# Performance work log

Measured on AMD Instinct MI355X. Metric: run time of the kernel, lower is better.

The kernel has to match this reference:

```python
import jax, jax.numpy as jnp
import numpy as np

FM = 64            # feature_maps
PASS_STEPS = 3
OUT_BITS = 16


def _linear(x, w, b):
    return x @ w + b


def _mlp(x, w1, b1, w2, b2):
    return _linear(jax.nn.relu(_linear(x, w1, b1)), w2, b2)


def setup_inputs() -> dict:
    key = jax.random.key(0)
    ks = jax.random.split(key, 20)
    VAR, CON, NNZ = 100000, 50000, 2000000

    def w(k, i, o):
        return jax.random.normal(k, (i, o), dtype=jnp.float32) * 0.05

    inp = {
        "row_idx": jax.random.randint(ks[0], (NNZ,), 0, VAR),
        "col_idx": jax.random.randint(ks[1], (NNZ,), 0, CON),
        "adj_vals": jax.random.normal(ks[2], (NNZ,), dtype=jnp.float32),
        "conditions_values": jax.random.normal(ks[3], (CON,), dtype=jnp.float32),
        "var_count": VAR,
        "const_count": CON,
        # prepare_cond: 1 -> 2*FM -> FM
        "pc_w1": w(ks[4], 1, 2 * FM), "pc_b1": jnp.zeros((2 * FM,), jnp.float32),
        "pc_w2": w(ks[5], 2 * FM, FM), "pc_b2": jnp.zeros((FM,), jnp.float32),
        # constraint_update: 2*FM -> 2*FM -> FM
        "cu_w1": w(ks[6], 2 * FM, 2 * FM), "cu_b1": jnp.zeros((2 * FM,), jnp.float32),
        "cu_w2": w(ks[7], 2 * FM, FM), "cu_b2": jnp.zeros((FM,), jnp.float32),
        # variable_update: 2*FM -> 2*FM -> FM
        "vu_w1": w(ks[8], 2 * FM, 2 * FM), "vu_b1": jnp.zeros((2 * FM,), jnp.float32),
        "vu_w2": w(ks[9], 2 * FM, FM), "vu_b2": jnp.zeros((FM,), jnp.float32),
        # output: FM -> 2*FM -> OUT_BITS
        "out_w1": w(ks[10], FM, 2 * FM), "out_b1": jnp.zeros((2 * FM,), jnp.float32),
        "out_w2": w(ks[11], 2 * FM, OUT_BITS), "out_b2": jnp.zeros((OUT_BITS,), jnp.float32),
    }
    return inp


def reference(row_idx, col_idx, adj_vals, conditions_values, var_count, const_count,
              pc_w1, pc_b1, pc_w2, pc_b2,
              cu_w1, cu_b1, cu_w2, cu_b2,
              vu_w1, vu_b1, vu_w2, vu_b2,
              out_w1, out_b1, out_w2, out_b2):
    vals = jnp.abs(adj_vals)                                   # [nnz]
    variables = jnp.ones((var_count, FM), dtype=jnp.float32)   # [V, FM]
    constraints = _mlp(conditions_values[:, None], pc_w1, pc_b1, pc_w2, pc_b2)  # [C, FM]

    for _ in range(PASS_STEPS):
        # var -> const: A^T @ variables  (gather rows, scatter-add to cols)
        v2c = jax.ops.segment_sum(vals[:, None] * variables[row_idx],
                                  col_idx, num_segments=const_count)   # [C, FM]
        constraints = _mlp(jnp.concatenate([constraints, v2c], axis=-1),
                           cu_w1, cu_b1, cu_w2, cu_b2)
        # const -> var: A @ constraints
        c2v = jax.ops.segment_sum(vals[:, None] * constraints[col_idx],
                                  row_idx, num_segments=var_count)     # [V, FM]
        variables = _mlp(jnp.concatenate([variables, c2v], axis=-1),
                         vu_w1, vu_b1, vu_w2, vu_b2)

    return jax.nn.sigmoid(_mlp(variables, out_w1, out_b1, out_w2, out_b2))  # [V, OUT_BITS]
```

## Files before the change

### kernel.cpp

```cpp
#include <hip/hip_runtime.h>
#include <hip/hip_fp16.h>

typedef unsigned int uint;

#define GB_D 64
#define MS_CH 8192
#define BS_CAP 6912

using h8  = __attribute__((ext_vector_type(8))) _Float16;
using h4  = __attribute__((ext_vector_type(4))) _Float16;
using f4v = __attribute__((ext_vector_type(4))) float;

__device__ __forceinline__ float4 ld4(const float* p) { return *reinterpret_cast<const float4*>(p); }
__device__ __forceinline__ void st4(float* p, float4 v) { *reinterpret_cast<float4*>(p) = v; }
__device__ __forceinline__ void fma4(float4& a, float s, const float4 w) {
    a.x = fmaf(s, w.x, a.x); a.y = fmaf(s, w.y, a.y);
    a.z = fmaf(s, w.z, a.z); a.w = fmaf(s, w.w, a.w);
}
__device__ __forceinline__ uint pk2(float a, float b) {
    __half2 h = __floats2half2_rn(a, b);
    return *reinterpret_cast<uint*>(&h);
}

__global__ __launch_bounds__(256) void k_bhist(const int* __restrict__ row, const int* __restrict__ col,
                                               int nnz, int* __restrict__ bcnt, int nbc, int nbt) {
    extern __shared__ int ls[];
    for (int b = threadIdx.x; b < nbt; b += blockDim.x) ls[b] = 0;
    __syncthreads();
    int i0 = blockIdx.x * blockDim.x + threadIdx.x;
    int stride = gridDim.x * blockDim.x;
    for (int i = i0; i < nnz; i += stride) {
        atomicAdd(&ls[col[i] >> 6], 1);
        atomicAdd(&ls[nbc + (row[i] >> 6)], 1);
    }
    __syncthreads();
    for (int b = threadIdx.x; b < nbt; b += blockDim.x) {
        int c = ls[b];
        if (c) atomicAdd(&bcnt[b], c);
    }
}

__global__ __launch_bounds__(1024) void k_bscan(const int* __restrict__ cnt, int n,
                                                int* __restrict__ ptr, int* __restrict__ nxt) {
    __shared__ int wsum[17];
    __shared__ int carry, tot;
    if (threadIdx.x == 0) carry = 0;
    __syncthreads();
    int lane = threadIdx.x & 63;
    int wid  = threadIdx.x >> 6;
    for (int base = 0; base < n; base += 1024) {
        int idx = base + (int)threadIdx.x;
        int v = (idx < n) ? cnt[idx] : 0;
        int inc = v;
        #pragma unroll
        for (int off = 1; off < 64; off <<= 1) {
            int t = __shfl_up(inc, (unsigned)off, 64);
            if (lane >= off) inc += t;
        }
        if (lane == 63) wsum[wid] = inc;
        __syncthreads();
        if (threadIdx.x == 0) {
            int s = 0;
            for (int w = 0; w < 16; w++) { int t = wsum[w]; wsum[w] = s; s += t; }
            tot = s;
        }
        __syncthreads();
        int excl = carry + wsum[wid] + (inc - v);
        if (idx < n) { ptr[idx] = excl; nxt[idx] = excl; }
        __syncthreads();
        if (threadIdx.x == 0) carry += tot;
        __syncthreads();
    }
    if (threadIdx.x == 0) ptr[n] = carry;
}

__global__ __launch_bounds__(256) void k_mpsplit(const int* __restrict__ row, const int* __restrict__ col,
                                                 const float* __restrict__ adj, int nnz,
                                                 int* __restrict__ bnxt, int2* __restrict__ pack,
                                                 int nbc, int nbt) {
    extern __shared__ int ls[];
    const int t = threadIdx.x;
    for (int b = t; b < nbt; b += 256) ls[b] = 0;
    __syncthreads();
    const int start = blockIdx.x * MS_CH;
    const int end = min(start + MS_CH, nnz);
    for (int i = start + t; i < end; i += 256) {
        atomicAdd(&ls[col[i] >> 6], 1);
        atomicAdd(&ls[nbc + (row[i] >> 6)], 1);
    }
    __syncthreads();
    for (int b = t; b < nbt; b += 256) {
        int c = ls[b];
        ls[b] = c ? atomicAdd(&bnxt[b], c) : 0;
    }
    __syncthreads();
    for (int i = start + t; i < end; i += 256) {
        int r = row[i], c = col[i];
        int vb = __float_as_int(fabsf(adj[i]));
        int p1 = atomicAdd(&ls[c >> 6], 1);
        pack[p1] = make_int2(((c & 63) << 20) | r, vb);
        int p2 = atomicAdd(&ls[nbc + (r >> 6)], 1);
        pack[p2] = make_int2(((r & 63) << 20) | c, vb);
    }
}

__global__ __launch_bounds__(256) void k_bsort(const int* __restrict__ bptr, int2* __restrict__ pack,
                                               int* __restrict__ dptr_c, int C,
                                               int* __restrict__ dptr_v, int V, int nbc) {
    __shared__ int2 ebuf[BS_CAP];
    __shared__ int h[GB_D];
    __shared__ int cur[GB_D];
    const int b = blockIdx.x, t = threadIdx.x;
    const int s = bptr[b], e = bptr[b + 1];
    const int n = min(e - s, BS_CAP);
    if (t < GB_D) h[t] = 0;
    __syncthreads();
    for (int i = t; i < n; i += 256) {
        int2 ed = pack[s + i];
        ebuf[i] = ed;
        atomicAdd(&h[((uint)ed.x) >> 20], 1);
    }
    __syncthreads();
    if (t < GB_D) {
        int v = h[t];
        int inc = v;
        #pragma unroll
        for (int off = 1; off < 64; off <<= 1) {
            int u = __shfl_up(inc, (unsigned)off, 64);
            if (t >= off) inc += u;
        }
        int excl = inc - v;
        cur[t] = excl;
        const bool isC = (b < nbc);
        const int base = (isC ? b : b - nbc) << 6;
        const int nd   = isC ? C : V;
        int* dp        = isC ? dptr_c : dptr_v;
        const int d = base + t;
        if (d < nd) dp[d] = s + excl;
        if (d == nd - 1) dp[nd] = s + n;
    }
    __syncthreads();
    for (int i = t; i < n; i += 256) {
        int2 ed = ebuf[i];
        int p = atomicAdd(&cur[((uint)ed.x) >> 20], 1);
        pack[s + p] = make_int2(ed.x & 0xFFFFF, ed.y);
    }
}

__global__ __launch_bounds__(256) void k_gather(const int* __restrict__ dptr,
                                                const int2* __restrict__ es,
                                                const __half* __restrict__ sfeat,
                                                float* __restrict__ dmsg, int n) {
    int wid = (int)((blockIdx.x * blockDim.x + threadIdx.x) >> 6);
    int lane = threadIdx.x & 63;
    int nw = (int)((gridDim.x * blockDim.x) >> 6);
    for (int d = wid; d < n; d += nw) {
        int s = dptr[d], e = dptr[d + 1];
        float a0 = 0.f, a1 = 0.f, a2 = 0.f, a3 = 0.f;
        float a4 = 0.f, a5 = 0.f, a6 = 0.f, a7 = 0.f;
        int i = s;
        for (; i + 7 < e; i += 8) {
            int2 e0 = es[i],     e1 = es[i + 1], e2 = es[i + 2], e3 = es[i + 3];
            int2 e4 = es[i + 4], e5 = es[i + 5], e6 = es[i + 6], e7 = es[i + 7];
            a0 = fmaf(__int_as_float(e0.y), __half2float(sfeat[(size_t)e0.x * 64 + lane]), a0);
            a1 = fmaf(__int_as_float(e1.y), __half2float(sfeat[(size_t)e1.x * 64 + lane]), a1);
            a2 = fmaf(__int_as_float(e2.y), __half2float(sfeat[(size_t)e2.x * 64 + lane]), a2);
            a3 = fmaf(__int_as_float(e3.y), __half2float(sfeat[(size_t)e3.x * 64 + lane]), a3);
            a4 = fmaf(__int_as_float(e4.y), __half2float(sfeat[(size_t)e4.x * 64 + lane]), a4);
            a5 = fmaf(__int_as_float(e5.y), __half2float(sfeat[(size_t)e5.x * 64 + lane]), a5);
            a6 = fmaf(__int_as_float(e6.y), __half2float(sfeat[(size_t)e6.x * 64 + lane]), a6);
            a7 = fmaf(__int_as_float(e7.y), __half2float(sfeat[(size_t)e7.x * 64 + lane]), a7);
        }
        for (; i + 1 < e; i += 2) {
            int2 e0 = es[i], e1 = es[i + 1];
            a0 = fmaf(__int_as_float(e0.y), __half2float(sfeat[(size_t)e0.x * 64 + lane]), a0);
            a1 = fmaf(__int_as_float(e1.y), __half2float(sfeat[(size_t)e1.x * 64 + lane]), a1);
        }
        if (i < e) {
            int2 e0 = es[i];
            a0 = fmaf(__int_as_float(e0.y), __half2float(sfeat[(size_t)e0.x * 64 + lane]), a0);
        }
        dmsg[(size_t)d * 64 + lane] = ((a0 + a1) + (a2 + a3)) + ((a4 + a5) + (a6 + a7));
    }
}

__global__ __launch_bounds__(256) void k_ones2(float4* p, int n4, uint4* ph, int n4h) {
    int i0 = blockIdx.x * blockDim.x + threadIdx.x;
    int stride = gridDim.x * blockDim.x;
    float4 one = make_float4(1.f, 1.f, 1.f, 1.f);
    uint4 oneh = make_uint4(0x3C003C00u, 0x3C003C00u, 0x3C003C00u, 0x3C003C00u);
    for (int i = i0; i < n4; i += stride) p[i] = one;
    for (int i = i0; i < n4h; i += stride) ph[i] = oneh;
}

__global__ __launch_bounds__(256) void k_pc2(const float* __restrict__ cond, float* __restrict__ constraints,
                                             __half* __restrict__ conh, int C,
                                             const float* __restrict__ w1, const float* __restrict__ b1,
                                             const float* __restrict__ w2, const float* __restrict__ b2) {
    __shared__ float hs[64][132];
    __shared__ float cs[64];
    const int t = threadIdx.x;
    const int base = blockIdx.x * 64;
    const int rem = C - base;

    if (t < 64) cs[t] = (t < rem) ? cond[base + t] : 0.f;
    __syncthreads();

    #pragma unroll
    for (int j = 0; j < 32; j++) {
        int idx = j * 256 + t;
        int k = idx & 127, row = idx >> 7;
        hs[row][k] = fmaxf(fmaf(cs[row], w1[k], b1[k]), 0.f);
    }
    __syncthreads();

    const int tx2 = t & 15, ty2 = t >> 4;
    float4 bb = ld4(b2 + tx2 * 4);
    float4 acc[4] = { bb, bb, bb, bb };
    const float* w2p = w2 + tx2 * 4;
    #pragma unroll 4
    for (int k = 0; k < 128; k++) {
        float4 w = ld4(w2p + k * 64);
        fma4(acc[0], hs[ty2 * 4 + 0][k], w);
        fma4(acc[1], hs[ty2 * 4 + 1][k], w);
        fma4(acc[2], hs[ty2 * 4 + 2][k], w);
        fma4(acc[3], hs[ty2 * 4 + 3][k], w);
    }
    #pragma unroll
    for (int r = 0; r < 4; r++) {
        int row = ty2 * 4 + r;
        if (row < rem) {
            st4(&constraints[(size_t)(base + row) * 64 + tx2 * 4], acc[r]);
            uint2 o;
            o.x = pk2(acc[r].x, acc[r].y);
            o.y = pk2(acc[r].z, acc[r].w);
            *(uint2*)(conh + (size_t)(base + row) * 64 + tx2 * 4) = o;
        }
    }
}

__global__ __launch_bounds__(256) void k_mlp3(float* __restrict__ feat, const float* __restrict__ msg,
                                              __half* __restrict__ mirror, int n,
                                              const float* __restrict__ w1, const float* __restrict__ b1,
                                              const float* __restrict__ w2, const float* __restrict__ b2) {
    __shared__ _Float16 xh[64][136];
    __shared__ _Float16 xl[64][136];
    const int t = threadIdx.x;
    const int base = blockIdx.x * 64;
    const int rem = n - base;
    const int wv = t >> 6;
    const int la = t & 15;
    const int lb = (t & 63) >> 4;

    {
        const float4* f4p = (const float4*)(feat + (size_t)base * 64);
        const float4* m4p = (const float4*)(msg + (size_t)base * 64);
        #pragma unroll
        for (int j = 0; j < 8; j++) {
            int idx = j * 256 + t;
            int row = idx >> 5;
            int q   = idx & 31;
            float4 v = make_float4(0.f, 0.f, 0.f, 0.f);
            if (row < rem) v = (q < 16) ? f4p[row * 16 + q] : m4p[row * 16 + (q - 16)];
            int k = (q < 16) ? q * 4 : 64 + (q - 16) * 4;
            h4 hi, lo;
            hi[0] = (_Float16)v.x; lo[0] = (_Float16)(v.x - (float)hi[0]);
            hi[1] = (_Float16)v.y; lo[1] = (_Float16)(v.y - (float)hi[1]);
            hi[2] = (_Float16)v.z; lo[2] = (_Float16)(v.z - (float)hi[2]);
            hi[3] = (_Float16)v.w; lo[3] = (_Float16)(v.w - (float)hi[3]);
            *(h4*)&xh[row][k] = hi;
            *(h4*)&xl[row][k] = lo;
        }
    }

    h8 B1[2][4];
    h8 B2[4];
    #pragma unroll
    for (int nn = 0; nn < 2; nn++) {
        int col = wv * 32 + nn * 16 + la;
        #pragma unroll
        for (int kc = 0; kc < 4; kc++) {
            int kb = kc * 32 + lb * 8;
            h8 bb;
            #pragma unroll
            for (int j = 0; j < 8; j++) bb[j] = (_Float16)w1[(kb + j) * 128 + col];
            B1[nn][kc] = bb;
        }
    }
    {
        int col = wv * 16 + la;
        #pragma unroll
        for (int kc = 0; kc < 4; kc++) {
            int kb = kc * 32 + lb * 8;
            h8 bb;
            #pragma unroll
            for (int j = 0; j < 8; j++) bb[j] = (_Float16)w2[(kb + j) * 64 + col];
            B2[kc] = bb;
        }
    }
    const float b1v0 = b1[wv * 32 + la];
    const float b1v1 = b1[wv * 32 + 16 + la];
    const float b2v  = b2[wv * 16 + la];

    __syncthreads();

    f4v acc[4][2];
    #pragma unroll
    for (int r = 0; r < 4; r++) {
        f4v z = {0.f, 0.f, 0.f, 0.f};
        acc[r][0] = z; acc[r][1] = z;
    }
    #pragma unroll
    for (int r = 0; r < 4; r++) {
        h8 Ah[4], Al[4];
        #pragma unroll
        for (int kc = 0; kc < 4; kc++) {
            Ah[kc] = *(const h8*)&xh[r * 16 + la][kc * 32 + lb * 8];
            Al[kc] = *(const h8*)&xl[r * 16 + la][kc * 32 + lb * 8];
        }
        #pragma unroll
        for (int nn = 0; nn < 2; nn++) {
            #pragma unroll
            for (int kc = 0; kc < 4; kc++) {
                acc[r][nn] = __builtin_amdgcn_mfma_f32_16x16x32_f16(Ah[kc], B1[nn][kc], acc[r][nn], 0, 0, 0);
                acc[r][nn] = __builtin_amdgcn_mfma_f32_16x16x32_f16(Al[kc], B1[nn][kc], acc[r][nn], 0, 0, 0);
            }
        }
    }
    __syncthreads();

    #pragma unroll
    for (int r = 0; r < 4; r++) {
        #pragma unroll
        for (int nn = 0; nn < 2; nn++) {
            const float bv = nn ? b1v1 : b1v0;
            const int col = wv * 32 + nn * 16 + la;
            #pragma unroll
            for (int i = 0; i < 4; i++) {
                float h = fmaxf(acc[r][nn][i] + bv, 0.f);
                int row = r * 16 + lb * 4 + i;
                _Float16 hh = (_Float16)h;
                xh[row][col] = hh;
                xl[row][col] = (_Float16)(h - (float)hh);
            }
        }
    }
    __syncthreads();

    f4v acc2[4];
    #pragma unroll
    for (int r = 0; r < 4; r++) { f4v z = {0.f, 0.f, 0.f, 0.f}; acc2[r] = z; }
    #pragma unroll
    for (int r = 0; r < 4; r++) {
        h8 Ah[4], Al[4];
        #pragma unroll
        for (int kc = 0; kc < 4; kc++) {
            Ah[kc] = *(const h8*)&xh[r * 16 + la][kc * 32 + lb * 8];
            Al[kc] = *(const h8*)&xl[r * 16 + la][kc * 32 + lb * 8];
        }
        #pragma unroll
        for (int kc = 0; kc < 4; kc++) {
            acc2[r] = __builtin_amdgcn_mfma_f32_16x16x32_f16(Ah[kc], B2[kc], acc2[r], 0, 0, 0);
            acc2[r] = __builtin_amdgcn_mfma_f32_16x16x32_f16(Al[kc], B2[kc], acc2[r], 0, 0, 0);
        }
    }

    {
        const int col = wv * 16 + la;
        #pragma unroll
        for (int r = 0; r < 4; r++) {
            #pragma unroll
            for (int i = 0; i < 4; i++) {
                int row = r * 16 + lb * 4 + i;
                if (row < rem) {
                    float y = acc2[r][i] + b2v;
                    size_t idx = (size_t)(base + row) * 64 + col;
                    feat[idx] = y;
                    mirror[idx] = __float2half_rn(y);
                }
            }
        }
    }
}

__global__ __launch_bounds__(256) void k_out3(const float* __restrict__ vars, float* __restrict__ out, int V,
                                              const float* __restrict__ w1, const float* __restrict__ b1,
                                              const float* __restrict__ w2, const float* __restrict__ b2) {
    __shared__ _Float16 xh[64][136];
    __shared__ _Float16 xl[64][136];
    const int t = threadIdx.x;
    const int base = blockIdx.x * 64;
    const int rem = V - base;
    const int wv = t >> 6;
    const int la = t & 15;
    const int lb = (t & 63) >> 4;

    {
        const float4* v4p = (const float4*)(vars + (size_t)base * 64);
        #pragma unroll
        for (int j = 0; j < 4; j++) {
            int idx = j * 256 + t;
            int row = idx >> 4;
            int q   = idx & 15;
            float4 v = make_float4(0.f, 0.f, 0.f, 0.f);
            if (row < rem) v = v4p[row * 16 + q];
            int k = q * 4;
            h4 hi, lo;
            hi[0] = (_Float16)v.x; lo[0] = (_Float16)(v.x - (float)hi[0]);
            hi[1] = (_Float16)v.y; lo[1] = (_Float16)(v.y - (float)hi[1]);
            hi[2] = (_Float16)v.z; lo[2] = (_Float16)(v.z - (float)hi[2]);
            hi[3] = (_Float16)v.w; lo[3] = (_Float16)(v.w - (float)hi[3]);
            *(h4*)&xh[row][k] = hi;
            *(h4*)&xl[row][k] = lo;
        }
    }

    h8 B1[2][2];
    h8 B2[4];
    #pragma unroll
    for (int nn = 0; nn < 2; nn++) {
        int col = wv * 32 + nn * 16 + la;
        #pragma unroll
        for (int kc = 0; kc < 2; kc++) {
            int kb = kc * 32 + lb * 8;
            h8 bb;
            #pragma unroll
            for (int j = 0; j < 8; j++) bb[j] = (_Float16)w1[(kb + j) * 128 + col];
            B1[nn][kc] = bb;
        }
    }
    {
        int col = la;
        #pragma unroll
        for (int kc = 0; kc < 4; kc++) {
            int kb = kc * 32 + lb * 8;
            h8 bb;
            #pragma unroll
            for (int j = 0; j < 8; j++) bb[j] = (_Float16)w2[(kb + j) * 16 + col];
            B2[kc] = bb;
        }
    }
    const float b1v0 = b1[wv * 32 + la];
    const float b1v1 = b1[wv * 32 + 16 + la];
    const float b2v  = b2[la];

    __syncthreads();

    f4v acc[4][2];
    #pragma unroll
    for (int r = 0; r < 4; r++) {
        f4v z = {0.f, 0.f, 0.f, 0.f};
        acc[r][0] = z; acc[r][1] = z;
    }
    #pragma unroll
    for (int r = 0; r < 4; r++) {
        h8 Ah[2], Al[2];
        #pragma unroll
        for (int kc = 0; kc < 2; kc++) {
            Ah[kc] = *(const h8*)&xh[r * 16 + la][kc * 32 + lb * 8];
            Al[kc] = *(const h8*)&xl[r * 16 + la][kc * 32 + lb * 8];
        }
        #pragma unroll
        for (int nn = 0; nn < 2; nn++) {
            #pragma unroll
            for (int kc = 0; kc < 2; kc++) {
                acc[r][nn] = __builtin_amdgcn_mfma_f32_16x16x32_f16(Ah[kc], B1[nn][kc], acc[r][nn], 0, 0, 0);
                acc[r][nn] = __builtin_amdgcn_mfma_f32_16x16x32_f16(Al[kc], B1[nn][kc], acc[r][nn], 0, 0, 0);
            }
        }
    }
    __syncthreads();

    #pragma unroll
    for (int r = 0; r < 4; r++) {
        #pragma unroll
        for (int nn = 0; nn < 2; nn++) {
            const float bv = nn ? b1v1 : b1v0;
            const int col = wv * 32 + nn * 16 + la;
            #pragma unroll
            for (int i = 0; i < 4; i++) {
                float h = fmaxf(acc[r][nn][i] + bv, 0.f);
                int row = r * 16 + lb * 4 + i;
                _Float16 hh = (_Float16)h;
                xh[row][col] = hh;
                xl[row][col] = (_Float16)(h - (float)hh);
            }
        }
    }
    __syncthreads();

    f4v acc2 = {0.f, 0.f, 0.f, 0.f};
    {
        h8 Ah[4], Al[4];
        #pragma unroll
        for (int kc = 0; kc < 4; kc++) {
            Ah[kc] = *(const h8*)&xh[wv * 16 + la][kc * 32 + lb * 8];
            Al[kc] = *(const h8*)&xl[wv * 16 + la][kc * 32 + lb * 8];
        }
        #pragma unroll
        for (int kc = 0; kc < 4; kc++) {
            acc2 = __builtin_amdgcn_mfma_f32_16x16x32_f16(Ah[kc], B2[kc], acc2, 0, 0, 0);
            acc2 = __builtin_amdgcn_mfma_f32_16x16x32_f16(Al[kc], B2[kc], acc2, 0, 0, 0);
        }
    }

    #pragma unroll
    for (int i = 0; i < 4; i++) {
        int row = wv * 16 + lb * 4 + i;
        if (row < rem) {
            float y = acc2[i] + b2v;
            out[(size_t)(base + row) * 16 + la] = 1.f / (1.f + __expf(-y));
        }
    }
}


extern "C" void kernel_launch(void* const* d_in, const int* in_sizes, int n_in,
                              void* d_out, int out_size, void* d_ws, size_t ws_size,
                              hipStream_t stream) {
    const int*   row_idx = (const int*)d_in[0];
    const int*   col_idx = (const int*)d_in[1];
    const float* adj     = (const float*)d_in[2];
    const float* cond    = (const float*)d_in[3];
    const float* pc_w1  = (const float*)d_in[6];
    const float* pc_b1  = (const float*)d_in[7];
    const float* pc_w2  = (const float*)d_in[8];
    const float* pc_b2  = (const float*)d_in[9];
    const float* cu_w1  = (const float*)d_in[10];
    const float* cu_b1  = (const float*)d_in[11];
    const float* cu_w2  = (const float*)d_in[12];
    const float* cu_b2  = (const float*)d_in[13];
    const float* vu_w1  = (const float*)d_in[14];
    const float* vu_b1  = (const float*)d_in[15];
    const float* vu_w2  = (const float*)d_in[16];
    const float* vu_b2  = (const float*)d_in[17];
    const float* out_w1 = (const float*)d_in[18];
    const float* out_b1 = (const float*)d_in[19];
    const float* out_w2 = (const float*)d_in[20];
    const float* out_b2 = (const float*)d_in[21];

    const int NNZ = in_sizes[0];
    const int C   = in_sizes[3];
    const int V   = out_size / 16;

    const int NBc = (C + GB_D - 1) / GB_D;
    const int NBv = (V + GB_D - 1) / GB_D;
    const int NBT = NBc + NBv;

    float* out = (float*)d_out;

    char* wsb = (char*)d_ws;
    size_t off = 0;
    auto carve = [&](size_t bytes) -> void* {
        void* p = wsb + off;
        off = (off + bytes + 255) & ~(size_t)255;
        return p;
    };
    float*  variables   = (float*)carve((size_t)V * 64 * 4);
    float*  constraints = (float*)carve((size_t)C * 64 * 4);
    float*  v2c         = (float*)carve((size_t)C * 64 * 4);
    float*  c2v         = (float*)carve((size_t)V * 64 * 4);
    __half* var_h       = (__half*)carve((size_t)V * 64 * 2);
    __half* con_h       = (__half*)carve((size_t)C * 64 * 2);
    int2*   pack        = (int2*)carve((size_t)2 * NNZ * 8);
    int*    bcnt        = (int*)carve((size_t)NBT * 4);
    int*    bptr        = (int*)carve((size_t)(NBT + 1) * 4);
    int*    bnxt        = (int*)carve((size_t)NBT * 4);
    int*    dptr_c      = (int*)carve((size_t)(C + 1) * 4);
    int*    dptr_v      = (int*)carve((size_t)(V + 1) * 4);
    (void)ws_size; (void)n_in;

    const size_t shmem = (size_t)NBT * 4;

    hipMemsetAsync(bcnt, 0, (size_t)NBT * 4, stream);
    k_bhist<<<256, 256, shmem, stream>>>(row_idx, col_idx, NNZ, bcnt, NBc, NBT);
    k_bscan<<<1, 1024, 0, stream>>>(bcnt, NBT, bptr, bnxt);
    k_mpsplit<<<(NNZ + MS_CH - 1) / MS_CH, 256, shmem, stream>>>(row_idx, col_idx, adj, NNZ,
                                                                 bnxt, pack, NBc, NBT);
    k_bsort<<<NBT, 256, 0, stream>>>(bptr, pack, dptr_c, C, dptr_v, V, NBc);

    k_ones2<<<2048, 256, 0, stream>>>((float4*)variables, V * 16, (uint4*)var_h, V * 8);
    k_pc2<<<(C + 63) / 64, 256, 0, stream>>>(cond, constraints, con_h, C, pc_w1, pc_b1, pc_w2, pc_b2);

    for (int p = 0; p < 3; p++) {
        k_gather<<<2048, 256, 0, stream>>>(dptr_c, pack, var_h, v2c, C);
        k_mlp3<<<(C + 63) / 64, 256, 0, stream>>>(constraints, v2c, con_h, C, cu_w1, cu_b1, cu_w2, cu_b2);
        k_gather<<<2048, 256, 0, stream>>>(dptr_v, pack, con_h, c2v, V);
        k_mlp3<<<(V + 63) / 64, 256, 0, stream>>>(variables, c2v, var_h, V, vu_w1, vu_b1, vu_w2, vu_b2);
    }

    k_out3<<<(V + 63) / 64, 256, 0, stream>>>(variables, out, V, out_w1, out_b1, out_w2, out_b2);
}
```

Measured before the change: 823.2 us.

## Skip first-pass v2c gather via row-sum of weights and drop ones init

Because the variables start as all ones, the first var-to-constraint message equals the per-constraint sum of |adj| weights. That sum is now computed inside the bucket-sort kernel and written straight into v2c, so the first gather and the ones-fill kernel are no longer needed. The variable-update MLP gets a flag that substitutes ones for the feature input on the first pass, and it skips the half-precision mirror write on the last pass. Histogram and offset atomics are also spread over 8 sub-counters per bucket to cut global atomic contention. The risk is extra shared-memory float atomics in the sort kernel and a different summation order for the first message.

After: 817.6 us. Within noise of the previous version (-0.7%).

```diff
diff --git a/kernel.cpp b/kernel.cpp
--- a/kernel.cpp
+++ b/kernel.cpp
@@ -5,6 +5,7 @@
 
 #define GB_D 64
 #define MS_CH 8192
+#define NG 8
 #define BS_CAP 6912
 
 using h8  = __attribute__((ext_vector_type(8))) _Float16;
@@ -25,18 +26,20 @@
 __global__ __launch_bounds__(256) void k_bhist(const int* __restrict__ row, const int* __restrict__ col,
                                                int nnz, int* __restrict__ bcnt, int nbc, int nbt) {
     extern __shared__ int ls[];
-    for (int b = threadIdx.x; b < nbt; b += blockDim.x) ls[b] = 0;
-    __syncthreads();
-    int i0 = blockIdx.x * blockDim.x + threadIdx.x;
-    int stride = gridDim.x * blockDim.x;
-    for (int i = i0; i < nnz; i += stride) {
+    const int t = threadIdx.x;
+    for (int b = t; b < nbt; b += 256) ls[b] = 0;
+    __syncthreads();
+    const int start = blockIdx.x * MS_CH;
+    const int end = min(start + MS_CH, nnz);
+    for (int i = start + t; i < end; i += 256) {
         atomicAdd(&ls[col[i] >> 6], 1);
         atomicAdd(&ls[nbc + (row[i] >> 6)], 1);
     }
     __syncthreads();
-    for (int b = threadIdx.x; b < nbt; b += blockDim.x) {
+    const int g = blockIdx.x & (NG - 1);
+    for (int b = t; b < nbt; b += 256) {
         int c = ls[b];
-        if (c) atomicAdd(&bcnt[b], c);
+        if (c) atomicAdd(&bcnt[b * NG + g], c);
     }
 }
 
@@ -89,9 +92,10 @@
         atomicAdd(&ls[nbc + (row[i] >> 6)], 1);
     }
     __syncthreads();
+    const int g = blockIdx.x & (NG - 1);
     for (int b = t; b < nbt; b += 256) {
         int c = ls[b];
-        ls[b] = c ? atomicAdd(&bnxt[b], c) : 0;
+        ls[b] = c ? atomicAdd(&bnxt[b * NG + g], c) : 0;
     }
     __syncthreads();
     for (int i = start + t; i < end; i += 256) {
@@ -106,21 +110,26 @@
 
 __global__ __launch_bounds__(256) void k_bsort(const int* __restrict__ bptr, int2* __restrict__ pack,
                                                int* __restrict__ dptr_c, int C,
-                                               int* __restrict__ dptr_v, int V, int nbc) {
+                                               int* __restrict__ dptr_v, int V, int nbc,
+                                               float* __restrict__ v2c) {
     __shared__ int2 ebuf[BS_CAP];
     __shared__ int h[GB_D];
     __shared__ int cur[GB_D];
+    __shared__ float sw[GB_D];
     const int b = blockIdx.x, t = threadIdx.x;
-    const int s = bptr[b], e = bptr[b + 1];
+    const int s = bptr[b * NG], e = bptr[(b + 1) * NG];
     const int n = min(e - s, BS_CAP);
-    if (t < GB_D) h[t] = 0;
+    if (t < GB_D) { h[t] = 0; sw[t] = 0.f; }
     __syncthreads();
     for (int i = t; i < n; i += 256) {
         int2 ed = pack[s + i];
         ebuf[i] = ed;
-        atomicAdd(&h[((uint)ed.x) >> 20], 1);
-    }
-    __syncthreads();
+        int d = ((uint)ed.x) >> 20;
+        atomicAdd(&h[d], 1);
+        atomicAdd(&sw[d], __int_as_float(ed.y));
+    }
+    __syncthreads();
+    const bool isC = (b < nbc);
     if (t < GB_D) {
         int v = h[t];
         int inc = v;
@@ -131,7 +140,6 @@
         }
         int excl = inc - v;
         cur[t] = excl;
-        const bool isC = (b < nbc);
         const int base = (isC ? b : b - nbc) << 6;
         const int nd   = isC ? C : V;
         int* dp        = isC ? dptr_c : dptr_v;
@@ -144,6 +152,18 @@
         int2 ed = ebuf[i];
         int p = atomicAdd(&cur[((uint)ed.x) >> 20], 1);
         pack[s + p] = make_int2(ed.x & 0xFFFFF, ed.y);
+    }
+    if (isC) {
+        const int dbase = b << 6;
+        #pragma unroll
+        for (int i = t; i < GB_D * 16; i += 256) {
+            int d = i >> 4;
+            int dd = dbase + d;
+            if (dd < C) {
+                float v = sw[d];
+                st4(&v2c[(size_t)dd * 64 + (i & 15) * 4], make_float4(v, v, v, v));
+            }
+        }
     }
 }
 
@@ -184,15 +204,6 @@
     }
 }
 
-__global__ __launch_bounds__(256) void k_ones2(float4* p, int n4, uint4* ph, int n4h) {
-    int i0 = blockIdx.x * blockDim.x + threadIdx.x;
-    int stride = gridDim.x * blockDim.x;
-    float4 one = make_float4(1.f, 1.f, 1.f, 1.f);
-    uint4 oneh = make_uint4(0x3C003C00u, 0x3C003C00u, 0x3C003C00u, 0x3C003C00u);
-    for (int i = i0; i < n4; i += stride) p[i] = one;
-    for (int i = i0; i < n4h; i += stride) ph[i] = oneh;
-}
-
 __global__ __launch_bounds__(256) void k_pc2(const float* __restrict__ cond, float* __restrict__ constraints,
                                              __half* __restrict__ conh, int C,
                                              const float* __restrict__ w1, const float* __restrict__ b1,
@@ -240,7 +251,7 @@
 }
 
 __global__ __launch_bounds__(256) void k_mlp3(float* __restrict__ feat, const float* __restrict__ msg,
-                                              __half* __restrict__ mirror, int n,
+                                              __half* __restrict__ mirror, int n, int feat_ones,
                                               const float* __restrict__ w1, const float* __restrict__ b1,
                                               const float* __restrict__ w2, const float* __restrict__ b2) {
     __shared__ _Float16 xh[64][136];
@@ -261,7 +272,10 @@
             int row = idx >> 5;
             int q   = idx & 31;
             float4 v = make_float4(0.f, 0.f, 0.f, 0.f);
-            if (row < rem) v = (q < 16) ? f4p[row * 16 + q] : m4p[row * 16 + (q - 16)];
+            if (row < rem) {
+                if (q < 16) v = feat_ones ? make_float4(1.f, 1.f, 1.f, 1.f) : f4p[row * 16 + q];
+                else        v = m4p[row * 16 + (q - 16)];
+            }
             int k = (q < 16) ? q * 4 : 64 + (q - 16) * 4;
             h4 hi, lo;
             hi[0] = (_Float16)v.x; lo[0] = (_Float16)(v.x - (float)hi[0]);
@@ -376,7 +390,7 @@
                     float y = acc2[r][i] + b2v;
                     size_t idx = (size_t)(base + row) * 64 + col;
                     feat[idx] = y;
-                    mirror[idx] = __float2half_rn(y);
+                    if (mirror) mirror[idx] = __float2half_rn(y);
                 }
             }
         }
@@ -546,6 +560,7 @@
     const int NBc = (C + GB_D - 1) / GB_D;
     const int NBv = (V + GB_D - 1) / GB_D;
     const int NBT = NBc + NBv;
+    const int NCH = (NNZ + MS_CH - 1) / MS_CH;
 
     float* out = (float*)d_out;
 
@@ -563,30 +578,33 @@
     __half* var_h       = (__half*)carve((size_t)V * 64 * 2);
     __half* con_h       = (__half*)carve((size_t)C * 64 * 2);
     int2*   pack        = (int2*)carve((size_t)2 * NNZ * 8);
-    int*    bcnt        = (int*)carve((size_t)NBT * 4);
-    int*    bptr        = (int*)carve((size_t)(NBT + 1) * 4);
-    int*    bnxt        = (int*)carve((size_t)NBT * 4);
+    int*    bcnt        = (int*)carve((size_t)NBT * NG * 4);
+    int*    bptr        = (int*)carve((size_t)(NBT * NG + 1) * 4);
+    int*    bnxt        = (int*)carve((size_t)(NBT * NG + 1) * 4);
     int*    dptr_c      = (int*)carve((size_t)(C + 1) * 4);
     int*    dptr_v      = (int*)carve((size_t)(V + 1) * 4);
     (void)ws_size; (void)n_in;
 
     const size_t shmem = (size_t)NBT * 4;
 
-    hipMemsetAsync(bcnt, 0, (size_t)NBT * 4, stream);
-    k_bhist<<<256, 256, shmem, stream>>>(row_idx, col_idx, NNZ, bcnt, NBc, NBT);
-    k_bscan<<<1, 1024, 0, stream>>>(bcnt, NBT, bptr, bnxt);
-    k_mpsplit<<<(NNZ + MS_CH - 1) / MS_CH, 256, shmem, stream>>>(row_idx, col_idx, adj, NNZ,
-                                                                 bnxt, pack, NBc, NBT);
-    k_bsort<<<NBT, 256, 0, stream>>>(bptr, pack, dptr_c, C, dptr_v, V, NBc);
-
-    k_ones2<<<2048, 256, 0, stream>>>((float4*)variables, V * 16, (uint4*)var_h, V * 8);
+    hipMemsetAsync(bcnt, 0, (size_t)NBT * NG * 4, stream);
+    k_bhist<<<NCH, 256, shmem, stream>>>(row_idx, col_idx, NNZ, bcnt, NBc, NBT);
+    k_bscan<<<1, 1024, 0, stream>>>(bcnt, NBT * NG, bptr, bnxt);
+    k_mpsplit<<<NCH, 256, shmem, stream>>>(row_idx, col_idx, adj, NNZ, bnxt, pack, NBc, NBT);
+    k_bsort<<<NBT, 256, 0, stream>>>(bptr, pack, dptr_c, C, dptr_v, V, NBc, v2c);
+
     k_pc2<<<(C + 63) / 64, 256, 0, stream>>>(cond, constraints, con_h, C, pc_w1, pc_b1, pc_w2, pc_b2);
 
     for (int p = 0; p < 3; p++) {
-        k_gather<<<2048, 256, 0, stream>>>(dptr_c, pack, var_h, v2c, C);
-        k_mlp3<<<(C + 63) / 64, 256, 0, stream>>>(constraints, v2c, con_h, C, cu_w1, cu_b1, cu_w2, cu_b2);
+        if (p > 0) {
+            k_gather<<<2048, 256, 0, stream>>>(dptr_c, pack, var_h, v2c, C);
+        }
+        k_mlp3<<<(C + 63) / 64, 256, 0, stream>>>(constraints, v2c, con_h, C, 0,
+                                                  cu_w1, cu_b1, cu_w2, cu_b2);
         k_gather<<<2048, 256, 0, stream>>>(dptr_v, pack, con_h, c2v, V);
-        k_mlp3<<<(V + 63) / 64, 256, 0, stream>>>(variables, c2v, var_h, V, vu_w1, vu_b1, vu_w2, vu_b2);
+        k_mlp3<<<(V + 63) / 64, 256, 0, stream>>>(variables, c2v,
+                                                  (p == 2) ? (__half*)nullptr : var_h, V, (p == 0) ? 1 : 0,
+                                                  vu_w1, vu_b1, vu_w2, vu_b2);
     }
 
     k_out3<<<(V + 63) / 64, 256, 0, stream>>>(variables, out, V, out_w1, out_b1, out_w2, out_b2);
```
